# Kernel optimization log

Measured on AMD Instinct MI355X. Metric: run time of the kernel, lower is better.

The kernel has to match this reference:

```python
import jax, jax.numpy as jnp
import numpy as np

SCALE = 2
STRIDE = 1


def setup_inputs() -> dict:
    key = jax.random.key(0)
    kx, kw, kb = jax.random.split(key, 3)
    B, Cin, H, W = 16, 128, 64, 64
    Cout, kh, kw_ = 128, 3, 3
    N = Cout * Cin * kh * kw_
    bound = 1.0 / np.sqrt(N)
    x = jax.random.normal(kx, (B, Cin, H, W), dtype=jnp.float32)
    weight = jax.random.uniform(kw, (Cout, Cin, kh, kw_), dtype=jnp.float32,
                                minval=-bound, maxval=bound)
    bias = jax.random.uniform(kb, (Cout,), dtype=jnp.float32,
                              minval=-bound, maxval=bound)
    return {"x": x, "weight": weight, "bias": bias}


def reference(x, weight, bias):
    # Nearest-neighbor upsample: each input pixel replicated SCALE x SCALE.
    up = jnp.repeat(jnp.repeat(x, SCALE, axis=2), SCALE, axis=3)  # [B,C,H*s,W*s]
    # Conv2d (cross-correlation, no padding), same math as unfold + matmul.
    out = jax.lax.conv_general_dilated(
        up, weight,
        window_strides=(STRIDE, STRIDE),
        padding="VALID",
        dimension_numbers=("NCHW", "OIHW", "NCHW"),
    )
    return out + bias[None, :, None, None]
```

## Files before the change

kernel.cpp:

```cpp
#include <hip/hip_runtime.h>
#include <hip/hip_bf16.h>
#include <stdint.h>


#define B_    16
#define CIN   128
#define HIN   64
#define WIN   64
#define COUT  128
#define HO    126
#define WO    126
#define BM    63
#define KTILES 16
#define AS_K  520

typedef __bf16 bf16;
typedef __bf16 bf16x8 __attribute__((ext_vector_type(8)));
typedef float  floatx4 __attribute__((ext_vector_type(4)));
typedef float  floatx2 __attribute__((ext_vector_type(2)));

__global__ void prep_weights(const float* __restrict__ w, bf16* __restrict__ wb) {
    int idx = blockIdx.x * 256 + threadIdx.x;
    if (idx >= 4 * KTILES * COUT * 32) return;
    int k32 = idx & 31;
    int o   = (idx >> 5) & 127;
    int par = (idx >> 12) & 3;
    int kt  = idx >> 14;
    int k = kt * 32 + k32;
    int c = k >> 2, u = (k >> 1) & 1, v = k & 1;
    int a = par >> 1, bp = par & 1;
    int dy0, dy1, ndy, dx0, dx1, ndx;
    if (u == 0) { if (a == 0) { dy0 = 0; dy1 = 1; ndy = 2; } else { dy0 = 0; dy1 = 0; ndy = 1; } }
    else        { if (a == 0) { dy0 = 2; dy1 = 2; ndy = 1; } else { dy0 = 1; dy1 = 2; ndy = 2; } }
    if (v == 0) { if (bp == 0) { dx0 = 0; dx1 = 1; ndx = 2; } else { dx0 = 0; dx1 = 0; ndx = 1; } }
    else        { if (bp == 0) { dx0 = 2; dx1 = 2; ndx = 1; } else { dx0 = 1; dx1 = 2; ndx = 2; } }
    const float* wp = w + (o * CIN + c) * 9;
    float s = wp[dy0 * 3 + dx0];
    if (ndx == 2) s += wp[dy0 * 3 + dx1];
    if (ndy == 2) { s += wp[dy1 * 3 + dx0]; if (ndx == 2) s += wp[dy1 * 3 + dx1]; }
    wb[idx] = (bf16)s;
}

__global__ __launch_bounds__(512, 4)
void upconv_gemm(const float* __restrict__ x, const bf16* __restrict__ wb,
                 const float* __restrict__ bias, float* __restrict__ out) {
    __shared__ bf16 As[64 * AS_K];
    floatx2* Ld2 = reinterpret_cast<floatx2*>(As);

    const int t    = threadIdx.x;
    const int lane = t & 63;
    const int wid  = t >> 6;
    const int a    = wid >> 2;
    const int oq   = wid & 3;
    const int quad = lane >> 4;
    const int l15  = lane & 15;
    const int kq   = quad * 8;

    const int bid = blockIdx.x;
    const int b   = bid / 63;
    const int p   = bid - b * 63;

    {
        const bool mvalid = (lane < 63);
        const float* xbase = x + ((b * CIN) * HIN + p) * WIN + lane;

        #pragma unroll
        for (int j = 0; j < 8; ++j) {
            const int c0 = wid * 16 + 2 * j;
            float f0[4] = {0.f, 0.f, 0.f, 0.f}, f1[4] = {0.f, 0.f, 0.f, 0.f};
            if (mvalid) {
                const float* pa = xbase + c0 * (HIN * WIN);
                f0[0] = pa[0]; f0[1] = pa[1]; f0[2] = pa[WIN]; f0[3] = pa[WIN + 1];
                const float* pb = pa + (HIN * WIN);
                f1[0] = pb[0]; f1[1] = pb[1]; f1[2] = pb[WIN]; f1[3] = pb[WIN + 1];
            }
            bf16x8 v;
            v[0] = (bf16)f0[0]; v[1] = (bf16)f0[1]; v[2] = (bf16)f0[2]; v[3] = (bf16)f0[3];
            v[4] = (bf16)f1[0]; v[5] = (bf16)f1[1]; v[6] = (bf16)f1[2]; v[7] = (bf16)f1[3];
            const int g = wid * 8 + j;
            *(bf16x8*)&As[lane * AS_K + g * 8] = v;
        }
    }
    __syncthreads();

    const bf16* wwave = wb + ((a * 2) * COUT + oq * 32 + l15) * 32 + kq;

    floatx4 acc[2][4][2] = {};

    #pragma unroll
    for (int kt = 0; kt < KTILES; ++kt) {
        bf16x8 af[4], wf[2][2];
        #pragma unroll
        for (int i = 0; i < 4; ++i)
            af[i] = *(const bf16x8*)&As[(i * 16 + l15) * AS_K + kt * 32 + kq];
        #pragma unroll
        for (int bp = 0; bp < 2; ++bp)
            #pragma unroll
            for (int nt = 0; nt < 2; ++nt)
                wf[bp][nt] = *(const bf16x8*)(wwave
                    + (kt * 4 * COUT + bp * COUT + nt * 16) * 32);
        #pragma unroll
        for (int bp = 0; bp < 2; ++bp)
            #pragma unroll
            for (int mt = 0; mt < 4; ++mt)
                #pragma unroll
                for (int nt = 0; nt < 2; ++nt)
                    acc[bp][mt][nt] = __builtin_amdgcn_mfma_f32_16x16x32_bf16(
                        wf[bp][nt], af[mt], acc[bp][mt][nt], 0, 0, 0);
    }

    float bv[2][4];
    #pragma unroll
    for (int nt = 0; nt < 2; ++nt)
        #pragma unroll
        for (int ri = 0; ri < 4; ++ri)
            bv[nt][ri] = bias[oq * 32 + nt * 16 + quad * 4 + ri];

    const int y0 = 2 * p;

    #pragma unroll
    for (int ap = 0; ap < 2; ++ap) {
        __syncthreads();

        if (a == ap) {
            #pragma unroll
            for (int mt = 0; mt < 4; ++mt)
                #pragma unroll
                for (int nt = 0; nt < 2; ++nt)
                    #pragma unroll
                    for (int ri = 0; ri < 4; ++ri) {
                        const int o = oq * 32 + nt * 16 + quad * 4 + ri;
                        const int q = mt * 16 + l15;
                        floatx2 r;
                        r[0] = acc[0][mt][nt][ri] + bv[nt][ri];
                        r[1] = acc[1][mt][nt][ri] + bv[nt][ri];
                        Ld2[o * 65 + q] = r;
                    }
        }
        __syncthreads();

        #pragma unroll
        for (int i = 0; i < 16; ++i) {
            const int o = wid * 16 + i;
            if (lane < 63) {
                floatx2 v = Ld2[o * 65 + lane];
                float* dst = out + ((b * COUT + o) * HO + (y0 + ap)) * WO + 2 * lane;
                __builtin_nontemporal_store(v, (floatx2*)dst);
            }
        }
    }
}

extern "C" void kernel_launch(void* const* d_in, const int* in_sizes, int n_in,
                              void* d_out, int out_size, void* d_ws, size_t ws_size,
                              hipStream_t stream) {
    const float* x    = (const float*)d_in[0];
    const float* w    = (const float*)d_in[1];
    const float* bias = (const float*)d_in[2];
    float* out = (float*)d_out;
    bf16* wb = (bf16*)d_ws;

    prep_weights<<<(4 * KTILES * COUT * 32 + 255) / 256, 256, 0, stream>>>(w, wb);

    upconv_gemm<<<dim3(B_ * 63), 512, 0, stream>>>(x, wb, bias, out);
}
```

Baseline: 212.4 us.

## Stage input rows through double-buffered LDS with global_load_lds

Replaces the per-lane scalar global loads of the 2x2 input patches with 16-byte global_load_lds transfers. Each chunk of 16 channels × 2 rows is copied into a double-buffered LDS staging area, then read back from LDS to build the bf16 A tile. This is meant to replace scattered, partly redundant 4-byte global reads with coalesced wide loads, and to overlap fetching the next chunk with packing the current one. The A tile shrinks to 63 rows, so the unused 64th row now reads staging memory instead of zeros. Those results are never stored, but the shared-memory footprint grows, and there are more barriers in the load phase.

```diff
diff --git a/kernel.cpp b/kernel.cpp
--- a/kernel.cpp
+++ b/kernel.cpp
@@ -10,9 +10,11 @@
 #define COUT  128
 #define HO    126
 #define WO    126
-#define BM    63
 #define KTILES 16
 #define AS_K  520
+#define AS_ROWS 63
+#define AS_BYTES (AS_ROWS * AS_K * 2)
+#define XS_BUF_F 2048
 
 typedef __bf16 bf16;
 typedef __bf16 bf16x8 __attribute__((ext_vector_type(8)));
@@ -44,8 +46,10 @@
 __global__ __launch_bounds__(512, 4)
 void upconv_gemm(const float* __restrict__ x, const bf16* __restrict__ wb,
                  const float* __restrict__ bias, float* __restrict__ out) {
-    __shared__ bf16 As[64 * AS_K];
-    floatx2* Ld2 = reinterpret_cast<floatx2*>(As);
+    __shared__ __align__(16) char smem[AS_BYTES + 2 * XS_BUF_F * 4];
+    bf16*  As  = (bf16*)smem;
+    float* Xs  = (float*)(smem + AS_BYTES);
+    floatx2* Ld2 = (floatx2*)smem;
 
     const int t    = threadIdx.x;
     const int lane = t & 63;
@@ -60,25 +64,33 @@
     const int b   = bid / 63;
     const int p   = bid - b * 63;
 
-    {
-        const bool mvalid = (lane < 63);
-        const float* xbase = x + ((b * CIN) * HIN + p) * WIN + lane;
+    const int cl = t >> 5;
+    const int rl = (t >> 4) & 1;
+    const int w4 = t & 15;
+    const float* gsrc = x + ((b * CIN + cl) * HIN + (p + rl)) * WIN + w4 * 4;
 
-        #pragma unroll
-        for (int j = 0; j < 8; ++j) {
-            const int c0 = wid * 16 + 2 * j;
-            float f0[4] = {0.f, 0.f, 0.f, 0.f}, f1[4] = {0.f, 0.f, 0.f, 0.f};
-            if (mvalid) {
-                const float* pa = xbase + c0 * (HIN * WIN);
-                f0[0] = pa[0]; f0[1] = pa[1]; f0[2] = pa[WIN]; f0[3] = pa[WIN + 1];
-                const float* pb = pa + (HIN * WIN);
-                f1[0] = pb[0]; f1[1] = pb[1]; f1[2] = pb[WIN]; f1[3] = pb[WIN + 1];
-            }
+    #define GLL_CHUNK(CH) \
+        __builtin_amdgcn_global_load_lds( \
+            (const __attribute__((address_space(1))) uint32_t*)(const void*)(gsrc + (CH) * 16 * HIN * WIN), \
+            (__attribute__((address_space(3))) uint32_t*)(void*)(Xs + ((CH) & 1) * XS_BUF_F + t * 4), \
+            16, 0, 0)
+
+    GLL_CHUNK(0);
+
+    #pragma unroll
+    for (int ch = 0; ch < 8; ++ch) {
+        __syncthreads();
+        if (ch < 7) GLL_CHUNK(ch + 1);
+        if (lane < 63) {
+            const float* Xb = Xs + (ch & 1) * XS_BUF_F + (2 * wid) * 128;
+            const float a00 = Xb[lane],       a01 = Xb[lane + 1];
+            const float a10 = Xb[64 + lane],  a11 = Xb[64 + lane + 1];
+            const float b00 = Xb[128 + lane], b01 = Xb[128 + lane + 1];
+            const float b10 = Xb[192 + lane], b11 = Xb[192 + lane + 1];
             bf16x8 v;
-            v[0] = (bf16)f0[0]; v[1] = (bf16)f0[1]; v[2] = (bf16)f0[2]; v[3] = (bf16)f0[3];
-            v[4] = (bf16)f1[0]; v[5] = (bf16)f1[1]; v[6] = (bf16)f1[2]; v[7] = (bf16)f1[3];
-            const int g = wid * 8 + j;
-            *(bf16x8*)&As[lane * AS_K + g * 8] = v;
+            v[0] = (bf16)a00; v[1] = (bf16)a01; v[2] = (bf16)a10; v[3] = (bf16)a11;
+            v[4] = (bf16)b00; v[5] = (bf16)b01; v[6] = (bf16)b10; v[7] = (bf16)b11;
+            *(bf16x8*)&As[lane * AS_K + (ch * 16 + 2 * wid) * 4] = v;
         }
     }
     __syncthreads();
```

Result: slower. 216.9 us (+2.1%).
